# Optimization experiments

Hardware: AMD Instinct MI355X
Metric: run time of the kernel (lower is better)

## Reference

```python
import jax, jax.numpy as jnp
import numpy as np
from jax import lax

INPUT_DIM = 1024
HIDDEN_DIM = 2048
N, L = 64, 512


def setup_inputs() -> dict:
    key = jax.random.key(0)
    ks = jax.random.split(key, 6)
    X = jax.random.normal(ks[0], (N, L, INPUT_DIM), dtype=jnp.float32)
    H0 = jnp.zeros((N, HIDDEN_DIM), dtype=jnp.float32)
    # G-invariant layer params (DeepSets invariant map): out = w * sum(x) + b, one per gate (i,f,g,o)
    inv_scale = 1.0 / np.sqrt(INPUT_DIM)
    inv_w = jax.random.normal(ks[1], (4, HIDDEN_DIM), dtype=jnp.float32) * inv_scale
    inv_b = jax.random.normal(ks[2], (4, HIDDEN_DIM), dtype=jnp.float32) * inv_scale
    # Linear(hidden, hidden) per gate, torch convention W: (out, in)
    lin_scale = 1.0 / np.sqrt(HIDDEN_DIM)
    lin_W = jax.random.normal(ks[3], (4, HIDDEN_DIM, HIDDEN_DIM), dtype=jnp.float32) * lin_scale
    lin_b = jax.random.normal(ks[4], (4, HIDDEN_DIM), dtype=jnp.float32) * lin_scale
    return {"X": X, "H0": H0, "inv_w": inv_w, "inv_b": inv_b, "lin_W": lin_W, "lin_b": lin_b}


def reference(X, H0, inv_w, inv_b, lin_W, lin_b):
    # X: (N, L, D); H0: (N, H)
    def step(carry, x_t):
        h, c = carry                               # (N, H), (N, H)
        s = jnp.sum(x_t, axis=-1, keepdims=True)   # (N, 1) invariant statistic
        inv = s * inv_w[:, None, :] + inv_b[:, None, :]            # (4, N, H)
        lin = jnp.einsum('nh,gkh->gnk', h, lin_W) + lin_b[:, None, :]  # (4, N, H)
        z = inv + lin
        i = jax.nn.sigmoid(z[0])
        f = jax.nn.sigmoid(z[1])
        g = jnp.tanh(z[2])
        o = jax.nn.sigmoid(z[3])
        c = f * c + i * g
        h = o * jnp.tanh(c)
        return (h, c), None

    Xt = jnp.swapaxes(X, 0, 1)                     # (L, N, D)
    (h, _), _ = lax.scan(step, (H0, jnp.zeros_like(H0)), Xt)
    # original returns swapdims(hidden_state, 0, 1) -> (H, N)
    return h.T
```

## Files before the change

kernel.cpp:

```cpp
#include <hip/hip_runtime.h>
#include <hip/hip_fp16.h>


typedef _Float16 f16x8 __attribute__((ext_vector_type(8)));
typedef float    f32x4 __attribute__((ext_vector_type(4)));
typedef unsigned long long u64;

static __device__ __forceinline__ float fast_sig(float x) {
  return 1.f / (1.f + __expf(-x));
}
static __device__ __forceinline__ float fast_tanh(float x) {
  x = fminf(15.f, fmaxf(-15.f, x));
  const float e = __expf(2.f * x);
  return (e - 1.f) / (e + 1.f);
}

static __device__ __forceinline__ void st_h16(void* p, float v) {
  const unsigned short b = __builtin_bit_cast(unsigned short, (_Float16)v);
  __hip_atomic_store((unsigned short*)p, b, __ATOMIC_RELAXED, __HIP_MEMORY_SCOPE_AGENT);
}
static __device__ __forceinline__ void st_h32(void* p, unsigned v) {
  __hip_atomic_store((unsigned*)p, v, __ATOMIC_RELAXED, __HIP_MEMORY_SCOPE_AGENT);
}

static __device__ __forceinline__ int h_off(int n, int j) {
  return ((n >> 4) << 16) + ((j >> 5) << 10) + ((n & 15) << 6) +
         (((j >> 3) & 3) << 4) + ((j & 7) << 1);
}

__global__ void __launch_bounds__(256) seq_sum_kernel(const float* __restrict__ X,
                                                      float* s_all) {
  const int gw   = (int)((blockIdx.x * blockDim.x + threadIdx.x) >> 6);
  const int lane = threadIdx.x & 63;
  const int n = gw >> 9, t = gw & 511;
  const float4* p = (const float4*)(X + ((size_t)gw << 10));
  float s = 0.f;
#pragma unroll
  for (int i = 0; i < 4; ++i) {
    const float4 v = p[lane + (i << 6)];
    s += (v.x + v.y) + (v.z + v.w);
  }
#pragma unroll
  for (int off = 32; off; off >>= 1) s += __shfl_xor(s, off);
  if (lane == 0) s_all[(t << 6) + n] = s;
}

__global__ void bar_init_kernel(unsigned* bar) {
  bar[threadIdx.x]       = 0u;
  bar[threadIdx.x + 256] = 0u;
  bar[threadIdx.x + 512] = 0u;
  bar[threadIdx.x + 768] = 0u;
}

static __device__ __forceinline__ void grid_barrier(unsigned* bar, unsigned round,
                                                    int tid, int blk) {
  asm volatile("s_waitcnt vmcnt(0)" ::: "memory");
  __syncthreads();
  if (tid == 0) {
    unsigned* base = bar + ((blk >> 7) << 8);
    unsigned* grp  = base + ((blk & 3) << 4);
    unsigned* root = base + 128;
    const unsigned old =
        __hip_atomic_fetch_add(grp, 1u, __ATOMIC_RELAXED, __HIP_MEMORY_SCOPE_AGENT);
    if (old == 32u * round - 1u)
      __hip_atomic_fetch_add(root, 1u, __ATOMIC_RELAXED, __HIP_MEMORY_SCOPE_AGENT);
    const unsigned target = round << 2;
    unsigned guard = 0;
    while (__hip_atomic_load(root, __ATOMIC_RELAXED, __HIP_MEMORY_SCOPE_AGENT) <
           target) {
      __builtin_amdgcn_s_sleep(1);
      if (++guard > (1u << 23)) break;
    }
  }
  __syncthreads();
}

#define LOAD4(d0, d1, d2, d3, addr)                                         \
  asm volatile("global_load_dwordx4 %0, %4, off sc1\n\t"                    \
               "global_load_dwordx4 %1, %4, off offset:1024 sc1\n\t"        \
               "global_load_dwordx4 %2, %4, off offset:2048 sc1\n\t"        \
               "global_load_dwordx4 %3, %4, off offset:3072 sc1"            \
               : "=&v"(d0), "=&v"(d1), "=&v"(d2), "=&v"(d3)                 \
               : "v"(addr)                                                  \
               : "memory")

#define WAITG4(n, A, b)                                                     \
  asm volatile("s_waitcnt vmcnt(" #n ")"                                    \
               : "+v"(A[(b)]), "+v"(A[(b) + 1]), "+v"(A[(b) + 2]),          \
                 "+v"(A[(b) + 3])                                           \
               :                                                            \
               : "memory")

#define KMATH4(A, b)                                                        \
  _Pragma("unroll")                                                         \
  for (int i_ = (b); i_ < (b) + 4; ++i_) {                                  \
    acc[0] = __builtin_amdgcn_mfma_f32_16x16x32_f16(A[i_], Wr[i_][0],       \
                                                    acc[0], 0, 0, 0);       \
    acc[1] = __builtin_amdgcn_mfma_f32_16x16x32_f16(A[i_], Wr[i_][1],       \
                                                    acc[1], 0, 0, 0);       \
    acc[2] = __builtin_amdgcn_mfma_f32_16x16x32_f16(A[i_], Wr[i_][2],       \
                                                    acc[2], 0, 0, 0);       \
    acc[3] = __builtin_amdgcn_mfma_f32_16x16x32_f16(A[i_], Wr[i_][3],       \
                                                    acc[3], 0, 0, 0);       \
  }

#define SCATTER(bt)                                                         \
  _Pragma("unroll")                                                         \
  for (int ct_ = 0; ct_ < 4; ++ct_) {                                       \
    const int kf_ = ct_ * 4 + (cc >> 2);                                    \
    _Pragma("unroll")                                                       \
    for (int v_ = 0; v_ < 4; ++v_) {                                        \
      const int n_  = (bt) * 16 + (q << 2) + v_;                            \
      const int key = (n_ & 15) ^ (n_ >> 4);                                \
      red[wave][n_][((kf_ ^ key) << 2) + (cc & 3)] = acc[ct_][v_];          \
    }                                                                       \
  }

__global__ void __launch_bounds__(256, 1) ginv_lstm_persist(
    const float* __restrict__ lin_W, const float* __restrict__ inv_w,
    const float* __restrict__ inv_b, const float* __restrict__ lin_b,
    const float* s_all, const float* __restrict__ H0,
    _Float16* hb0, _Float16* hb1, unsigned* bar, float* out) {
  __shared__ __align__(16) float s_lds[512][32];
  __shared__ __align__(16) float red[4][32][64];
  const int blk = blockIdx.x;
  const int tid = threadIdx.x;
  _Float16* hbuf[2] = {hb0, hb1};

  const int fblk = blk & 127;
  const int nh   = blk >> 7;

  const int wave = tid >> 6;
  const int lane = tid & 63;
  const int q    = lane >> 4;
  const int cc   = lane & 15;

  f16x8 Wr[16][4];
#pragma unroll
  for (int ct = 0; ct < 4; ++ct) {
    const int kf = ct * 4 + (cc >> 2), g = cc & 3;
    const float* wrow =
        lin_W + (((size_t)(g * 2048 + fblk * 16 + kf)) << 11) + wave * 512 + q * 8;
#pragma unroll
    for (int kc = 0; kc < 16; ++kc) {
      const float4 va = *(const float4*)(wrow + kc * 32);
      const float4 vb = *(const float4*)(wrow + kc * 32 + 4);
      f16x8 f;
      f[0] = (_Float16)va.x; f[1] = (_Float16)va.y;
      f[2] = (_Float16)va.z; f[3] = (_Float16)va.w;
      f[4] = (_Float16)vb.x; f[5] = (_Float16)vb.y;
      f[6] = (_Float16)vb.z; f[7] = (_Float16)vb.w;
      Wr[kc][ct] = f;
    }
  }

  {
    int i0 = blk * 512 + tid;
    st_h16((char*)hb0 + h_off(i0 >> 11, i0 & 2047), H0[i0]);
    i0 += 256;
    st_h16((char*)hb0 + h_off(i0 >> 11, i0 & 2047), H0[i0]);
  }

  for (int i = tid; i < 512 * 8; i += 256) {
    const int t4 = i >> 3, nl4 = (i & 7) << 2;
    *(float4*)&s_lds[t4][nl4] =
        *(const float4*)&s_all[(t4 << 6) + (nh << 5) + nl4];
  }

  const int nloc = (wave << 3) + (lane >> 3);
  const int c0   = (lane & 7) << 1;
  float iw[2][4], ibb[2][4];
#pragma unroll
  for (int kk = 0; kk < 2; ++kk) {
    const int Kg = fblk * 16 + c0 + kk;
#pragma unroll
    for (int g = 0; g < 4; ++g) {
      iw[kk][g]  = inv_w[(g << 11) + Kg];
      ibb[kk][g] = inv_b[(g << 11) + Kg] + lin_b[(g << 11) + Kg];
    }
  }

  unsigned round = 1;
  grid_barrier(bar, round, tid, blk);

  float cst[2] = {0.f, 0.f};
  float hnew[2] = {0.f, 0.f};

  const int ld_base = ((nh * 2) << 16) + (wave << 14) + (cc << 6) + (q << 4);
  const int hst_off = ((nh * 2 + (nloc >> 4)) << 16) + ((fblk >> 1) << 10) +
                      ((nloc & 15) << 6) + ((fblk & 1) << 5) + (c0 << 1);
  const int key = (nloc & 15) ^ (nloc >> 4);

  for (int t = 0; t < 512; ++t) {
    const char* hpb = (const char*)hbuf[t & 1] + ld_base;

    f16x8 pa[16], pb[16];
    f32x4 acc[4];

#pragma unroll
    for (int w = 0; w < 4; ++w)
      LOAD4(pa[w * 4], pa[w * 4 + 1], pa[w * 4 + 2], pa[w * 4 + 3],
            hpb + (w << 12));
#pragma unroll
    for (int w = 0; w < 4; ++w)
      LOAD4(pb[w * 4], pb[w * 4 + 1], pb[w * 4 + 2], pb[w * 4 + 3],
            hpb + 65536 + (w << 12));

#pragma unroll
    for (int ct = 0; ct < 4; ++ct) acc[ct] = (f32x4){0.f, 0.f, 0.f, 0.f};
    WAITG4(28, pa, 0);  KMATH4(pa, 0);
    WAITG4(24, pa, 4);  KMATH4(pa, 4);
    WAITG4(20, pa, 8);  KMATH4(pa, 8);
    WAITG4(16, pa, 12); KMATH4(pa, 12);
    SCATTER(0);

#pragma unroll
    for (int ct = 0; ct < 4; ++ct) acc[ct] = (f32x4){0.f, 0.f, 0.f, 0.f};
    WAITG4(12, pb, 0);  KMATH4(pb, 0);
    WAITG4(8,  pb, 4);  KMATH4(pb, 4);
    WAITG4(4,  pb, 8);  KMATH4(pb, 8);
    WAITG4(0,  pb, 12); KMATH4(pb, 12);
    SCATTER(1);

    __syncthreads();

    const float sv = s_lds[t][nloc];
#pragma unroll
    for (int kk = 0; kk < 2; ++kk) {
      const int off = ((c0 + kk) ^ key) << 2;
      f32x4 zz = *(const f32x4*)&red[0][nloc][off];
#pragma unroll
      for (int w = 1; w < 4; ++w) zz += *(const f32x4*)&red[w][nloc][off];
      const float zi = zz[0] + sv * iw[kk][0] + ibb[kk][0];
      const float zf = zz[1] + sv * iw[kk][1] + ibb[kk][1];
      const float zg = zz[2] + sv * iw[kk][2] + ibb[kk][2];
      const float zo = zz[3] + sv * iw[kk][3] + ibb[kk][3];
      const float ig = fast_sig(zi);
      const float fg = fast_sig(zf);
      const float gg = fast_tanh(zg);
      const float og = fast_sig(zo);
      const float cn = fg * cst[kk] + ig * gg;
      cst[kk] = cn;
      hnew[kk] = og * fast_tanh(cn);
    }

    {
      const unsigned lo = __builtin_bit_cast(unsigned short, (_Float16)hnew[0]);
      const unsigned hi = __builtin_bit_cast(unsigned short, (_Float16)hnew[1]);
      st_h32((char*)hbuf[(t + 1) & 1] + hst_off, lo | (hi << 16));
    }
    ++round;
    grid_barrier(bar, round, tid, blk);
  }

#pragma unroll
  for (int kk = 0; kk < 2; ++kk)
    out[((fblk * 16 + c0 + kk) << 6) + (nh << 5) + nloc] = hnew[kk];
}

extern "C" void kernel_launch(void* const* d_in, const int* in_sizes, int n_in,
                              void* d_out, int out_size, void* d_ws, size_t ws_size,
                              hipStream_t stream) {
  const float* X     = (const float*)d_in[0];
  const float* H0    = (const float*)d_in[1];
  const float* inv_w = (const float*)d_in[2];
  const float* inv_b = (const float*)d_in[3];
  const float* lin_W = (const float*)d_in[4];
  const float* lin_b = (const float*)d_in[5];
  float* out = (float*)d_out;

  const size_t S_BYTES = 512 * 64 * 4;
  const size_t BAR_PAD = 4096;
  const size_t H_BYTES = 64 * 2048 * 2;
  const size_t NEED = S_BYTES + BAR_PAD + 2 * H_BYTES;

  float*    s_all;
  unsigned* bar;
  _Float16* hb[2];
  if (ws_size >= NEED) {
    char* ws = (char*)d_ws;
    s_all = (float*)ws;
    bar   = (unsigned*)(ws + S_BYTES);
    for (int i = 0; i < 2; ++i)
      hb[i] = (_Float16*)(ws + S_BYTES + BAR_PAD + (size_t)i * H_BYTES);
  } else {
    s_all = (float*)d_out;
    char* xt = (char*)d_in[0] + (size_t)64 * 512 * 1024 * 4 -
               (BAR_PAD + 2 * H_BYTES);
    bar = (unsigned*)xt;
    for (int i = 0; i < 2; ++i)
      hb[i] = (_Float16*)(xt + BAR_PAD + (size_t)i * H_BYTES);
  }

  seq_sum_kernel<<<8192, 256, 0, stream>>>(X, s_all);
  bar_init_kernel<<<1, 256, 0, stream>>>(bar);
  ginv_lstm_persist<<<256, 256, 0, stream>>>(lin_W, inv_w, inv_b, lin_b, s_all, H0,
                                             hb[0], hb[1], bar, out);
}
```

Baseline: 3.897 ms.

## Replace grid barrier with per-wave sector counters and double-buffered reduction LDS

Removes the two-level grid barrier after each timestep. Each wave now bumps a per-sector counter after storing its h slice, and before loading, each wave polls only the counter for the h sector it reads. The reduction LDS is double-buffered so the missing end-of-step block sync does not cause overwrite hazards, and H0 is written using the same layout as the per-step stores. This cuts the barrier latency and lets waves proceed as soon as their inputs are ready, at the cost of more atomic traffic and polling on counters.

```diff
diff --git a/kernel.cpp b/kernel.cpp
--- a/kernel.cpp
+++ b/kernel.cpp
@@ -15,17 +15,8 @@
   return (e - 1.f) / (e + 1.f);
 }
 
-static __device__ __forceinline__ void st_h16(void* p, float v) {
-  const unsigned short b = __builtin_bit_cast(unsigned short, (_Float16)v);
-  __hip_atomic_store((unsigned short*)p, b, __ATOMIC_RELAXED, __HIP_MEMORY_SCOPE_AGENT);
-}
 static __device__ __forceinline__ void st_h32(void* p, unsigned v) {
   __hip_atomic_store((unsigned*)p, v, __ATOMIC_RELAXED, __HIP_MEMORY_SCOPE_AGENT);
-}
-
-static __device__ __forceinline__ int h_off(int n, int j) {
-  return ((n >> 4) << 16) + ((j >> 5) << 10) + ((n & 15) << 6) +
-         (((j >> 3) & 3) << 4) + ((j & 7) << 1);
 }
 
 __global__ void __launch_bounds__(256) seq_sum_kernel(const float* __restrict__ X,
@@ -50,29 +41,6 @@
   bar[threadIdx.x + 256] = 0u;
   bar[threadIdx.x + 512] = 0u;
   bar[threadIdx.x + 768] = 0u;
-}
-
-static __device__ __forceinline__ void grid_barrier(unsigned* bar, unsigned round,
-                                                    int tid, int blk) {
-  asm volatile("s_waitcnt vmcnt(0)" ::: "memory");
-  __syncthreads();
-  if (tid == 0) {
-    unsigned* base = bar + ((blk >> 7) << 8);
-    unsigned* grp  = base + ((blk & 3) << 4);
-    unsigned* root = base + 128;
-    const unsigned old =
-        __hip_atomic_fetch_add(grp, 1u, __ATOMIC_RELAXED, __HIP_MEMORY_SCOPE_AGENT);
-    if (old == 32u * round - 1u)
-      __hip_atomic_fetch_add(root, 1u, __ATOMIC_RELAXED, __HIP_MEMORY_SCOPE_AGENT);
-    const unsigned target = round << 2;
-    unsigned guard = 0;
-    while (__hip_atomic_load(root, __ATOMIC_RELAXED, __HIP_MEMORY_SCOPE_AGENT) <
-           target) {
-      __builtin_amdgcn_s_sleep(1);
-      if (++guard > (1u << 23)) break;
-    }
-  }
-  __syncthreads();
 }
 
 #define LOAD4(d0, d1, d2, d3, addr)                                         \
@@ -112,7 +80,7 @@
     for (int v_ = 0; v_ < 4; ++v_) {                                        \
       const int n_  = (bt) * 16 + (q << 2) + v_;                            \
       const int key = (n_ & 15) ^ (n_ >> 4);                                \
-      red[wave][n_][((kf_ ^ key) << 2) + (cc & 3)] = acc[ct_][v_];          \
+      rr[wave][n_][((kf_ ^ key) << 2) + (cc & 3)] = acc[ct_][v_];           \
     }                                                                       \
   }
 
@@ -122,7 +90,7 @@
     const float* s_all, const float* __restrict__ H0,
     _Float16* hb0, _Float16* hb1, unsigned* bar, float* out) {
   __shared__ __align__(16) float s_lds[512][32];
-  __shared__ __align__(16) float red[4][32][64];
+  __shared__ __align__(16) float red[2][4][32][64];
   const int blk = blockIdx.x;
   const int tid = threadIdx.x;
   _Float16* hbuf[2] = {hb0, hb1};
@@ -134,6 +102,9 @@
   const int lane = tid & 63;
   const int q    = lane >> 4;
   const int cc   = lane & 15;
+
+  unsigned* my_sector  = bar + (nh << 8) + ((fblk >> 5) << 4);
+  unsigned* rd_sector  = bar + (nh << 8) + (wave << 4);
 
   f16x8 Wr[16][4];
 #pragma unroll
@@ -154,13 +125,6 @@
     }
   }
 
-  {
-    int i0 = blk * 512 + tid;
-    st_h16((char*)hb0 + h_off(i0 >> 11, i0 & 2047), H0[i0]);
-    i0 += 256;
-    st_h16((char*)hb0 + h_off(i0 >> 11, i0 & 2047), H0[i0]);
-  }
-
   for (int i = tid; i < 512 * 8; i += 256) {
     const int t4 = i >> 3, nl4 = (i & 7) << 2;
     *(float4*)&s_lds[t4][nl4] =
@@ -180,19 +144,38 @@
     }
   }
 
-  unsigned round = 1;
-  grid_barrier(bar, round, tid, blk);
-
-  float cst[2] = {0.f, 0.f};
-  float hnew[2] = {0.f, 0.f};
-
   const int ld_base = ((nh * 2) << 16) + (wave << 14) + (cc << 6) + (q << 4);
   const int hst_off = ((nh * 2 + (nloc >> 4)) << 16) + ((fblk >> 1) << 10) +
                       ((nloc & 15) << 6) + ((fblk & 1) << 5) + (c0 << 1);
   const int key = (nloc & 15) ^ (nloc >> 4);
 
+  {
+    const float* h0p = H0 + ((nh << 5) + nloc) * 2048 + (fblk << 4) + c0;
+    const unsigned lo = __builtin_bit_cast(unsigned short, (_Float16)h0p[0]);
+    const unsigned hi = __builtin_bit_cast(unsigned short, (_Float16)h0p[1]);
+    st_h32((char*)hb0 + hst_off, lo | (hi << 16));
+  }
+  asm volatile("s_waitcnt vmcnt(0)" ::: "memory");
+  if ((tid & 63) == 0)
+    __hip_atomic_fetch_add(my_sector, 1u, __ATOMIC_RELAXED,
+                           __HIP_MEMORY_SCOPE_AGENT);
+
+  float cst[2] = {0.f, 0.f};
+  float hnew[2] = {0.f, 0.f};
+
   for (int t = 0; t < 512; ++t) {
+    {
+      const unsigned target = (unsigned)(t + 1) << 7;
+      unsigned guard = 0;
+      while (__hip_atomic_load(rd_sector, __ATOMIC_RELAXED,
+                               __HIP_MEMORY_SCOPE_AGENT) < target) {
+        __builtin_amdgcn_s_sleep(1);
+        if (++guard > (1u << 23)) break;
+      }
+    }
+
     const char* hpb = (const char*)hbuf[t & 1] + ld_base;
+    float (*rr)[32][64] = red[t & 1];
 
     f16x8 pa[16], pb[16];
     f32x4 acc[4];
@@ -228,9 +211,9 @@
 #pragma unroll
     for (int kk = 0; kk < 2; ++kk) {
       const int off = ((c0 + kk) ^ key) << 2;
-      f32x4 zz = *(const f32x4*)&red[0][nloc][off];
-#pragma unroll
-      for (int w = 1; w < 4; ++w) zz += *(const f32x4*)&red[w][nloc][off];
+      f32x4 zz = *(const f32x4*)&rr[0][nloc][off];
+#pragma unroll
+      for (int w = 1; w < 4; ++w) zz += *(const f32x4*)&rr[w][nloc][off];
       const float zi = zz[0] + sv * iw[kk][0] + ibb[kk][0];
       const float zf = zz[1] + sv * iw[kk][1] + ibb[kk][1];
       const float zg = zz[2] + sv * iw[kk][2] + ibb[kk][2];
@@ -249,8 +232,10 @@
       const unsigned hi = __builtin_bit_cast(unsigned short, (_Float16)hnew[1]);
       st_h32((char*)hbuf[(t + 1) & 1] + hst_off, lo | (hi << 16));
     }
-    ++round;
-    grid_barrier(bar, round, tid, blk);
+    asm volatile("s_waitcnt vmcnt(0)" ::: "memory");
+    if ((tid & 63) == 0)
+      __hip_atomic_fetch_add(my_sector, 1u, __ATOMIC_RELAXED,
+                             __HIP_MEMORY_SCOPE_AGENT);
   }
 
 #pragma unroll
```

Measured after the change: 13.04 ms. +234.6%, slower.
